# Performance work log

Measured on AMD Instinct MI355X. Metric: run time of the kernel, lower is better.

The kernel has to match this reference:

```python
import jax, jax.numpy as jnp
import numpy as np

DIM = 64
WIDTH = 128
INPUT_DIM = 16
N_NODES = 50000
N_EDGES = 100000
N_GRAPHS = 2500
STEPS = 5


def setup_inputs() -> dict:
    key = jax.random.key(0)
    ks = jax.random.split(key, 24)
    d = DIM
    def nrm(i, shape, fan_in):
        return jax.random.normal(ks[i], shape, jnp.float32) / np.float32(np.sqrt(fan_in))
    return {
        "x": jax.random.normal(ks[0], (N_NODES, INPUT_DIM - 1), jnp.float32),
        "z": jax.random.normal(ks[1], (N_NODES,), jnp.float32),
        "edge_attr": jax.random.uniform(ks[2], (N_EDGES, 5), jnp.float32),
        "lin0_w": nrm(3, (INPUT_DIM, d), INPUT_DIM),
        "lin0_b": jnp.zeros((d,), jnp.float32),
        "emlp_w1": nrm(4, (5, WIDTH), 5),
        "emlp_b1": jnp.zeros((WIDTH,), jnp.float32),
        "emlp_w2": nrm(5, (WIDTH, d * d), WIDTH),
        "emlp_b2": jnp.zeros((d * d,), jnp.float32),
        "conv_root": nrm(6, (d, d), d),
        "conv_bias": jnp.zeros((d,), jnp.float32),
        "gru_wi": nrm(7, (3 * d, d), d),
        "gru_wh": nrm(8, (3 * d, d), d),
        "gru_bi": jnp.zeros((3 * d,), jnp.float32),
        "gru_bh": jnp.zeros((3 * d,), jnp.float32),
        "lstm_wi": nrm(9, (4 * d, 2 * d), 2 * d),
        "lstm_wh": nrm(10, (4 * d, d), d),
        "lstm_bi": jnp.zeros((4 * d,), jnp.float32),
        "lstm_bh": jnp.zeros((4 * d,), jnp.float32),
        "lin1_w": nrm(11, (2 * d, d), 2 * d),
        "lin1_b": jnp.zeros((d,), jnp.float32),
        "lin2_w": nrm(12, (d, 1), d),
        "lin2_b": jnp.zeros((1,), jnp.float32),
        "edge_index": jax.random.randint(ks[13], (2, N_EDGES), 0, N_NODES),
        "batch": jnp.sort(jax.random.randint(ks[14], (N_NODES,), 0, N_GRAPHS)),
        "num_graphs": N_GRAPHS,
    }


def reference(x, z, edge_attr, lin0_w, lin0_b, emlp_w1, emlp_b1, emlp_w2, emlp_b2,
              conv_root, conv_bias, gru_wi, gru_wh, gru_bi, gru_bh,
              lstm_wi, lstm_wh, lstm_bi, lstm_bh, lin1_w, lin1_b, lin2_w, lin2_b,
              edge_index, batch, num_graphs):
    d = lin0_w.shape[1]
    n = x.shape[0]
    src, dst = edge_index[0], edge_index[1]
    # lin0 on [x | z]
    out = jax.nn.relu(jnp.concatenate([x, z[:, None]], axis=-1) @ lin0_w + lin0_b)  # [N, d]
    h = out
    # edge MLP -> per-edge weight matrix [E, d, d] (edge_attr fixed, compute once)
    ew = (jax.nn.relu(edge_attr @ emlp_w1 + emlp_b1) @ emlp_w2 + emlp_b2).reshape(-1, d, d)
    deg = jax.ops.segment_sum(jnp.ones_like(src, jnp.float32), dst, num_segments=n)
    denom = jnp.maximum(deg, 1.0)[:, None]
    for _ in range(STEPS):
        # NNConv: gather-matmul-scatter(mean) + root transform + bias
        msg = jnp.einsum('ei,eio->eo', out[src], ew)  # [E, d]
        aggr = jax.ops.segment_sum(msg, dst, num_segments=n) / denom
        m = jax.nn.relu(aggr + out @ conv_root + conv_bias)
        # GRU cell (torch gate order r, z, n)
        gi = m @ gru_wi.T + gru_bi
        gh = h @ gru_wh.T + gru_bh
        i_r, i_z, i_n = jnp.split(gi, 3, axis=-1)
        h_r, h_z, h_n = jnp.split(gh, 3, axis=-1)
        r = jax.nn.sigmoid(i_r + h_r)
        zg = jax.nn.sigmoid(i_z + h_z)
        ng = jnp.tanh(i_n + r * h_n)
        h = (1.0 - zg) * ng + zg * h
        out = h
    # Set2Set pooling (LSTM(2d -> d), torch gate order i, f, g, o)
    B = num_graphs
    q_star = jnp.zeros((B, 2 * d), out.dtype)
    hh = jnp.zeros((B, d), out.dtype)
    cc = jnp.zeros((B, d), out.dtype)
    for _ in range(STEPS):
        g = q_star @ lstm_wi.T + lstm_bi + hh @ lstm_wh.T + lstm_bh
        gi_, gf_, gg_, go_ = jnp.split(g, 4, axis=-1)
        cc = jax.nn.sigmoid(gf_) * cc + jax.nn.sigmoid(gi_) * jnp.tanh(gg_)
        hh = jax.nn.sigmoid(go_) * jnp.tanh(cc)
        q = hh
        e = jnp.sum(out * q[batch], axis=-1)  # [N]
        emax = jax.ops.segment_max(e, batch, num_segments=B)
        a = jnp.exp(e - emax[batch])
        asum = jax.ops.segment_sum(a, batch, num_segments=B) + 1e-16
        a = a / asum[batch]
        r_pool = jax.ops.segment_sum(a[:, None] * out, batch, num_segments=B)  # [B, d]
        q_star = jnp.concatenate([q, r_pool], axis=-1)
    y = jax.nn.relu(q_star @ lin1_w + lin1_b) @ lin2_w + lin2_b
    return y.reshape(-1)
```

## Files before the change

kernel.cpp:

```cpp
#include <hip/hip_runtime.h>
#include <hip/hip_bf16.h>

#define NN 50000
#define NE 100000
#define NG 2500
#define WW 128
#define EPAD 100096
#define KCH 264

typedef _Float16 h8 __attribute__((ext_vector_type(8)));
typedef _Float16 h4 __attribute__((ext_vector_type(4)));
typedef float    f4 __attribute__((ext_vector_type(4)));

#define GLOAD_LDS16(g, l) __builtin_amdgcn_global_load_lds( \
    (const __attribute__((address_space(1))) void*)(g),     \
    (__attribute__((address_space(3))) void*)(l), 16, 0, 0)

__device__ __forceinline__ float sigf(float x) { return 1.0f / (1.0f + __expf(-x)); }

__global__ void k_zero4(float4* __restrict__ p, int n4) {
    int i = blockIdx.x * 256 + threadIdx.x;
    if (i < n4) p[i] = make_float4(0.f, 0.f, 0.f, 0.f);
}

__global__ void k_transpose(float* dst, const float* src, int rows, int cols) {
    int idx = blockIdx.x * 256 + threadIdx.x;
    if (idx >= rows * cols) return;
    int r = idx / cols, c = idx % cols;
    dst[c * rows + r] = src[idx];
}

__global__ void k_lin0(const float* __restrict__ x, const float* __restrict__ z,
                       const float* __restrict__ w, const float* __restrict__ b,
                       float* __restrict__ s) {
    int idx = blockIdx.x * 256 + threadIdx.x;
    int n = idx >> 6, o = idx & 63;
    float acc = b[o];
#pragma unroll
    for (int i = 0; i < 15; i++) acc += x[n * 15 + i] * w[i * 64 + o];
    acc += z[n] * w[15 * 64 + o];
    s[idx] = fmaxf(acc, 0.0f);
}

__global__ void k_deg(const int* __restrict__ dstI, float* __restrict__ deg) {
    int e = blockIdx.x * 256 + threadIdx.x;
    if (e < NE) atomicAdd(&deg[dstI[e]], 1.0f);
}

__global__ void k_s16(const float* __restrict__ s, _Float16* __restrict__ s16) {
    int i = blockIdx.x * 256 + threadIdx.x;
    float4 v = ((const float4*)s)[i];
    h4 o = { (_Float16)v.x, (_Float16)v.y, (_Float16)v.z, (_Float16)v.w };
    *((h4*)s16 + i) = o;
}

__global__ void k_gstart(const int* __restrict__ batch, int* __restrict__ gstart) {
    int n = blockIdx.x * 256 + threadIdx.x;
    if (n > NN) return;
    int b1 = (n < NN) ? batch[n] : NG;
    int b0 = (n == 0) ? -1 : batch[n - 1];
    for (int g = b0 + 1; g <= b1; g++) gstart[g] = n;
}

__global__ void k_emlp_t(const float* __restrict__ ea, const float* __restrict__ w1,
                         const float* __restrict__ b1, _Float16* __restrict__ hidT) {
    __shared__ _Float16 hl[132][64];
    int t = threadIdx.x;
    int e0 = blockIdx.x * 64;
    int e_l = t & 63, w = t >> 6;
    int e = e0 + e_l;
    float a0 = 0, a1 = 0, a2 = 0, a3 = 0, a4 = 0;
    if (e < NE) {
        a0 = ea[e * 5 + 0]; a1 = ea[e * 5 + 1]; a2 = ea[e * 5 + 2];
        a3 = ea[e * 5 + 3]; a4 = ea[e * 5 + 4];
    }
    for (int h = w * 32; h < w * 32 + 32; h++) {
        float acc = b1[h];
        acc += a0 * w1[0 * 128 + h] + a1 * w1[1 * 128 + h] + a2 * w1[2 * 128 + h]
             + a3 * w1[3 * 128 + h] + a4 * w1[4 * 128 + h];
        hl[h][e_l] = (_Float16)fmaxf(acc, 0.0f);
    }
    if (t < 64) hl[128][t] = (_Float16)1.0f;
    else if (t < 128) hl[129][t - 64] = (_Float16)0.0f;
    else if (t < 192) hl[130][t - 128] = (_Float16)0.0f;
    else hl[131][t - 192] = (_Float16)0.0f;
    __syncthreads();
#pragma unroll
    for (int it = 0; it < 33; it++) {
        int idx = it * 256 + t;
        int h = idx >> 6, el = idx & 63;
        hidT[(size_t)h * EPAD + e0 + el] = hl[h][el];
    }
}

__global__ void k_prep_B(const float* __restrict__ w2, const float* __restrict__ b2,
                         _Float16* __restrict__ Bp) {
    int g = blockIdx.x * 256 + threadIdx.x;
    int l = g & 63, tt = (g >> 6) & 3, c = g >> 8;
    int n = tt * 16 + (l & 15);
    int kb = c * 32 + (l >> 4) * 8;
    h8 v;
#pragma unroll
    for (int j = 0; j < 8; j++) {
        int k = kb + j;
        float f = 0.0f;
        if (k < 8192) f = w2[(size_t)k * 64 + n];
        else if (k < 8256) f = b2[(k - 8192) * 64 + n];
        v[j] = (_Float16)f;
    }
    *((h8*)Bp + g) = v;
}

__global__ void k_prep_W(const float* __restrict__ conv_root,
                         const float* __restrict__ gru_wi,
                         const float* __restrict__ gru_wh,
                         _Float16* __restrict__ Bw) {
    int g = blockIdx.x * 256 + threadIdx.x;
    if (g >= 56 * 64) return;
    int l = g & 63, unit = g >> 6;
    int kb = ((unit & 1) * 32) + (l >> 4) * 8;
    h8 v;
    if (unit < 8) {
        int nt = unit >> 1;
        int n = nt * 16 + (l & 15);
#pragma unroll
        for (int j = 0; j < 8; j++) v[j] = (_Float16)conv_root[(kb + j) * 64 + n];
    } else if (unit < 32) {
        int nt = (unit - 8) >> 1;
        int o = nt * 16 + (l & 15);
#pragma unroll
        for (int j = 0; j < 8; j++) v[j] = (_Float16)gru_wi[o * 64 + kb + j];
    } else {
        int nt = (unit - 32) >> 1;
        int o = nt * 16 + (l & 15);
#pragma unroll
        for (int j = 0; j < 8; j++) v[j] = (_Float16)gru_wh[o * 64 + kb + j];
    }
    *((h8*)Bw + g) = v;
}

__global__ __launch_bounds__(128, 2) void k_fused(
        const _Float16* __restrict__ s16, const _Float16* __restrict__ hidT,
        const _Float16* __restrict__ Bp, const int* __restrict__ srcI,
        const int* __restrict__ dstI, float* __restrict__ aggr) {
    __shared__ uint4 Bl[2048];
    __shared__ _Float16 hle[128][4];
    int t = threadIdx.x, w = t >> 6, lane = t & 63;
    int m = lane & 15, q = lane >> 4;
    int e_blk = blockIdx.x * 128;
    int ew0 = e_blk + w * 64;

    h8 sA[4][2];
#pragma unroll
    for (int mt = 0; mt < 4; mt++) {
        int e = ew0 + mt * 16 + m;
        int src = (e < NE) ? srcI[e] : 0;
        const _Float16* sp = s16 + (size_t)src * 64;
        sA[mt][0] = *(const h8*)(sp + q * 8);
        sA[mt][1] = *(const h8*)(sp + 32 + q * 8);
    }
    f4 acc[4][4];
#pragma unroll
    for (int mt = 0; mt < 4; mt++)
#pragma unroll
        for (int nt = 0; nt < 4; nt++) acc[mt][nt] = (f4){0.f, 0.f, 0.f, 0.f};

    for (int sc = 0; sc < 33; sc++) {
        __syncthreads();
        const uint4* bsrc = (const uint4*)Bp + (size_t)sc * 2048;
#pragma unroll
        for (int r = 0; r < 16; r++) {
            int idx = r * 128 + t;
            GLOAD_LDS16(bsrc + idx, Bl + idx);
        }
        {
            const _Float16* hp = hidT + (size_t)(sc * 4) * EPAD + e_blk + t;
            h4 hv4;
            hv4[0] = hp[0];
            hv4[1] = hp[EPAD];
            hv4[2] = hp[2 * (size_t)EPAD];
            hv4[3] = hp[3 * (size_t)EPAD];
            *(h4*)&hle[t][0] = hv4;
        }
        __syncthreads();
        h4 hf[4];
#pragma unroll
        for (int mt = 0; mt < 4; mt++)
            hf[mt] = *(const h4*)&hle[w * 64 + mt * 16 + m][0];
#pragma unroll
        for (int cc = 0; cc < 8; cc++) {
            h8 b0 = *(const h8*)&Bl[(cc * 4 + 0) * 64 + lane];
            h8 b1 = *(const h8*)&Bl[(cc * 4 + 1) * 64 + lane];
            h8 b2 = *(const h8*)&Bl[(cc * 4 + 2) * 64 + lane];
            h8 b3 = *(const h8*)&Bl[(cc * 4 + 3) * 64 + lane];
            int hi = cc >> 1, kh = cc & 1;
#pragma unroll
            for (int mt = 0; mt < 4; mt++) {
                h8 a = sA[mt][kh] * hf[mt][hi];
                acc[mt][0] = __builtin_amdgcn_mfma_f32_16x16x32_f16(a, b0, acc[mt][0], 0, 0, 0);
                acc[mt][1] = __builtin_amdgcn_mfma_f32_16x16x32_f16(a, b1, acc[mt][1], 0, 0, 0);
                acc[mt][2] = __builtin_amdgcn_mfma_f32_16x16x32_f16(a, b2, acc[mt][2], 0, 0, 0);
                acc[mt][3] = __builtin_amdgcn_mfma_f32_16x16x32_f16(a, b3, acc[mt][3], 0, 0, 0);
            }
        }
    }
#pragma unroll
    for (int mt = 0; mt < 4; mt++) {
        int eb = ew0 + mt * 16 + q * 4;
#pragma unroll
        for (int r = 0; r < 4; r++) {
            int e = eb + r;
            if (e < NE) {
                int d = dstI[e];
                float* ap = aggr + (size_t)d * 64 + m;
                atomicAdd(ap + 0,  acc[mt][0][r]);
                atomicAdd(ap + 16, acc[mt][1][r]);
                atomicAdd(ap + 32, acc[mt][2][r]);
                atomicAdd(ap + 48, acc[mt][3][r]);
            }
        }
    }
}

__global__ __launch_bounds__(256) void k_combine2(
        float* __restrict__ s, _Float16* __restrict__ s16,
        const float* __restrict__ aggr, const float* __restrict__ deg,
        const _Float16* __restrict__ Bw, const float* __restrict__ cb,
        const float* __restrict__ bi, const float* __restrict__ bh) {
    __shared__ _Float16 ml[4][16][72];
    int t = threadIdx.x, w = t >> 6, lane = t & 63;
    int m = lane & 15, q = lane >> 4;
    int nb = blockIdx.x * 64 + w * 16;

    h8 sa0, sa1;
    {
        int node = nb + m; if (node >= NN) node = NN - 1;
        const _Float16* sp = s16 + (size_t)node * 64;
        sa0 = *(const h8*)(sp + q * 8);
        sa1 = *(const h8*)(sp + 32 + q * 8);
    }
    const h8* BW = (const h8*)Bw;

    f4 X[4], GH[12];
#pragma unroll
    for (int nt = 0; nt < 4; nt++) {
        X[nt] = (f4){0.f, 0.f, 0.f, 0.f};
        X[nt] = __builtin_amdgcn_mfma_f32_16x16x32_f16(sa0, BW[(nt * 2 + 0) * 64 + lane], X[nt], 0, 0, 0);
        X[nt] = __builtin_amdgcn_mfma_f32_16x16x32_f16(sa1, BW[(nt * 2 + 1) * 64 + lane], X[nt], 0, 0, 0);
    }
#pragma unroll
    for (int nt = 0; nt < 12; nt++) {
        GH[nt] = (f4){0.f, 0.f, 0.f, 0.f};
        GH[nt] = __builtin_amdgcn_mfma_f32_16x16x32_f16(sa0, BW[(32 + nt * 2 + 0) * 64 + lane], GH[nt], 0, 0, 0);
        GH[nt] = __builtin_amdgcn_mfma_f32_16x16x32_f16(sa1, BW[(32 + nt * 2 + 1) * 64 + lane], GH[nt], 0, 0, 0);
    }
#pragma unroll
    for (int r = 0; r < 4; r++) {
        int node = nb + q * 4 + r; if (node >= NN) node = NN - 1;
        float dn = fmaxf(deg[node], 1.0f);
#pragma unroll
        for (int nt = 0; nt < 4; nt++) {
            int o = nt * 16 + m;
            float mv = X[nt][r] + aggr[(size_t)node * 64 + o] / dn + cb[o];
            ml[w][q * 4 + r][o] = (_Float16)fmaxf(mv, 0.0f);
        }
    }
    __syncthreads();
    h8 ma0 = *(const h8*)&ml[w][m][q * 8];
    h8 ma1 = *(const h8*)&ml[w][m][32 + q * 8];

    f4 GI[12];
#pragma unroll
    for (int nt = 0; nt < 12; nt++) {
        GI[nt] = (f4){0.f, 0.f, 0.f, 0.f};
        GI[nt] = __builtin_amdgcn_mfma_f32_16x16x32_f16(ma0, BW[(8 + nt * 2 + 0) * 64 + lane], GI[nt], 0, 0, 0);
        GI[nt] = __builtin_amdgcn_mfma_f32_16x16x32_f16(ma1, BW[(8 + nt * 2 + 1) * 64 + lane], GI[nt], 0, 0, 0);
    }
#pragma unroll
    for (int og = 0; og < 4; og++) {
        int o = og * 16 + m;
        float bir = bi[o],       bhr = bh[o];
        float biz = bi[64 + o],  bhz = bh[64 + o];
        float bin = bi[128 + o], bhn = bh[128 + o];
#pragma unroll
        for (int r = 0; r < 4; r++) {
            int node = nb + q * 4 + r;
            if (node >= NN) continue;
            float rr = sigf(GI[og][r] + bir + GH[og][r] + bhr);
            float zz = sigf(GI[4 + og][r] + biz + GH[4 + og][r] + bhz);
            float ng = tanhf(GI[8 + og][r] + bin + rr * (GH[8 + og][r] + bhn));
            float hold = s[(size_t)node * 64 + o];
            float hnew = (1.0f - zz) * ng + zz * hold;
            s[(size_t)node * 64 + o] = hnew;
            s16[(size_t)node * 64 + o] = (_Float16)hnew;
        }
    }
}

__global__ void k_s2s(float* __restrict__ q_star, float* __restrict__ hh,
                      float* __restrict__ cc, const float* __restrict__ LiT,
                      const float* __restrict__ LhT, const float* __restrict__ bi,
                      const float* __restrict__ bh, const float* __restrict__ s,
                      const int* __restrict__ gstart, float* __restrict__ e_v) {
    __shared__ float qs[128], hv[64], g[256], qn[64];
    int b = blockIdx.x, t = threadIdx.x;
    if (t < 128) qs[t] = q_star[b * 128 + t];
    else if (t < 192) hv[t - 128] = hh[b * 64 + t - 128];
    __syncthreads();
    float acc = bi[t] + bh[t];
    for (int k = 0; k < 128; k++) acc += qs[k] * LiT[k * 256 + t];
    for (int k = 0; k < 64; k++) acc += hv[k] * LhT[k * 256 + t];
    g[t] = acc;
    __syncthreads();
    if (t < 64) {
        float c_new = sigf(g[64 + t]) * cc[b * 64 + t] + sigf(g[t]) * tanhf(g[128 + t]);
        cc[b * 64 + t] = c_new;
        float hq = sigf(g[192 + t]) * tanhf(c_new);
        hh[b * 64 + t] = hq;
        qn[t] = hq;
        q_star[b * 128 + t] = hq;
    }
    __syncthreads();
    if (t >= 64) return;
    int o = t;
    int n0 = gstart[b], n1 = gstart[b + 1];
    float q = qn[o];
    float mx = -3.4e38f;
    for (int n = n0; n < n1; n++) {
        float v = s[(size_t)n * 64 + o] * q;
#pragma unroll
        for (int off = 32; off; off >>= 1) v += __shfl_xor(v, off, 64);
        if (o == 0) e_v[n] = v;
        mx = fmaxf(mx, v);
    }
    float asum = 0.0f, rp = 0.0f;
    for (int n = n0; n < n1; n++) {
        float a = __expf(e_v[n] - mx);
        asum += a;
        rp += a * s[(size_t)n * 64 + o];
    }
    q_star[b * 128 + 64 + o] = rp / (asum + 1e-16f);
}

__global__ void k_final(const float* __restrict__ q_star, const float* __restrict__ w1,
                        const float* __restrict__ b1, const float* __restrict__ w2,
                        const float* __restrict__ b2, float* __restrict__ y) {
    __shared__ float qs[128];
    int b = blockIdx.x, t = threadIdx.x;
    qs[t] = q_star[b * 128 + t];
    qs[64 + t] = q_star[b * 128 + 64 + t];
    __syncthreads();
    float acc = b1[t];
    for (int k = 0; k < 128; k++) acc += qs[k] * w1[k * 64 + t];
    float hid = fmaxf(acc, 0.0f) * w2[t];
#pragma unroll
    for (int off = 32; off; off >>= 1) hid += __shfl_down(hid, off, 64);
    if (t == 0) y[b] = hid + b2[0];
}

static inline void zero_f(float* p, size_t nfloats, hipStream_t stream) {
    int n4 = (int)(nfloats / 4);
    k_zero4<<<(n4 + 255) / 256, 256, 0, stream>>>((float4*)p, n4);
}

extern "C" void kernel_launch(void* const* d_in, const int* in_sizes, int n_in,
                              void* d_out, int out_size, void* d_ws, size_t ws_size,
                              hipStream_t stream) {
    const float* x       = (const float*)d_in[0];
    const float* z       = (const float*)d_in[1];
    const float* ea      = (const float*)d_in[2];
    const float* lin0_w  = (const float*)d_in[3];
    const float* lin0_b  = (const float*)d_in[4];
    const float* emlp_w1 = (const float*)d_in[5];
    const float* emlp_b1 = (const float*)d_in[6];
    const float* emlp_w2 = (const float*)d_in[7];
    const float* emlp_b2 = (const float*)d_in[8];
    const float* conv_r  = (const float*)d_in[9];
    const float* conv_b  = (const float*)d_in[10];
    const float* gru_wi  = (const float*)d_in[11];
    const float* gru_wh  = (const float*)d_in[12];
    const float* gru_bi  = (const float*)d_in[13];
    const float* gru_bh  = (const float*)d_in[14];
    const float* lstm_wi = (const float*)d_in[15];
    const float* lstm_wh = (const float*)d_in[16];
    const float* lstm_bi = (const float*)d_in[17];
    const float* lstm_bh = (const float*)d_in[18];
    const float* lin1_w  = (const float*)d_in[19];
    const float* lin1_b  = (const float*)d_in[20];
    const float* lin2_w  = (const float*)d_in[21];
    const float* lin2_b  = (const float*)d_in[22];
    const int* eidx      = (const int*)d_in[23];
    const int* batch     = (const int*)d_in[24];
    const int* srcI = eidx;
    const int* dstI = eidx + NE;
    float* y = (float*)d_out;

    char* w = (char*)d_ws;
    size_t off = 0;
    auto alloc = [&](size_t bytes) -> void* {
        void* p = w + off;
        off += (bytes + 255) & ~(size_t)255;
        return p;
    };
    float* s      = (float*)alloc((size_t)NN * 64 * 4);
    float* aggr   = (float*)alloc((size_t)NN * 64 * 4);
    float* deg    = (float*)alloc((size_t)NN * 4);
    float* e_v    = (float*)alloc((size_t)NN * 4);
    float* q_star = (float*)alloc((size_t)NG * 128 * 4);
    float* hh     = (float*)alloc((size_t)NG * 64 * 4);
    float* cc     = (float*)alloc((size_t)NG * 64 * 4);
    float* LiT    = (float*)alloc(256 * 128 * 4);
    float* LhT    = (float*)alloc(256 * 64 * 4);
    int*   gstart = (int*)alloc((size_t)(NG + 1) * 4);
    _Float16* s16 = (_Float16*)alloc((size_t)NN * 64 * 2);
    _Float16* hidT= (_Float16*)alloc((size_t)132 * EPAD * 2);
    _Float16* Bp  = (_Float16*)alloc((size_t)KCH * 4 * 64 * 8 * 2);
    _Float16* Bw  = (_Float16*)alloc((size_t)56 * 64 * 8 * 2);
    (void)ws_size;

    k_transpose<<<(256 * 128 + 255) / 256, 256, 0, stream>>>(LiT, lstm_wi, 256, 128);
    k_transpose<<<(256 * 64 + 255) / 256, 256, 0, stream>>>(LhT, lstm_wh, 256, 64);
    k_prep_W<<<14, 256, 0, stream>>>(conv_r, gru_wi, gru_wh, Bw);

    k_lin0<<<NN * 64 / 256, 256, 0, stream>>>(x, z, lin0_w, lin0_b, s);
    k_s16<<<NN * 16 / 256, 256, 0, stream>>>(s, s16);
    zero_f(deg, NN, stream);
    k_deg<<<(NE + 255) / 256, 256, 0, stream>>>(dstI, deg);
    k_gstart<<<(NN + 256) / 256, 256, 0, stream>>>(batch, gstart);
    k_emlp_t<<<EPAD / 64, 256, 0, stream>>>(ea, emlp_w1, emlp_b1, hidT);
    k_prep_B<<<KCH * 4 * 64 / 256, 256, 0, stream>>>(emlp_w2, emlp_b2, Bp);

    for (int step = 0; step < 5; step++) {
        zero_f(aggr, (size_t)NN * 64, stream);
        k_fused<<<EPAD / 128, 128, 0, stream>>>(s16, hidT, Bp, srcI, dstI, aggr);
        k_combine2<<<(NN + 63) / 64, 256, 0, stream>>>(s, s16, aggr, deg, Bw,
                                                       conv_b, gru_bi, gru_bh);
    }

    zero_f(q_star, (size_t)NG * 128 + NG * 64 + NG * 64, stream);
    for (int it = 0; it < 5; it++) {
        k_s2s<<<NG, 256, 0, stream>>>(q_star, hh, cc, LiT, LhT, lstm_bi, lstm_bh,
                                      s, gstart, e_v);
    }
    k_final<<<NG, 64, 0, stream>>>(q_star, lin1_w, lin1_b, lin2_w, lin2_b, y);
}
```

Measured before the change: 1.056 ms.

## Double-buffer edge-weight B tiles in LDS and load hidden features directly as packed h4

The fused edge-conv kernel now splits each 2048-entry B chunk into two 1024-entry halves held in a double-buffered LDS array. The next half's global-to-LDS copy is issued before computing on the current half, overlapping memory transfer with MFMA work, and one barrier per half replaces two per chunk. The edge-MLP hidden activations are stored interleaved as h4 groups of four hidden units per edge, so each lane reads its own h4 straight from global memory, prefetched one step ahead. This removes the LDS staging buffer and an extra barrier. The costs are more registers for the prefetched values and a change in the hidT layout.

```diff
diff --git a/kernel.cpp b/kernel.cpp
--- a/kernel.cpp
+++ b/kernel.cpp
@@ -63,7 +63,7 @@
 }
 
 __global__ void k_emlp_t(const float* __restrict__ ea, const float* __restrict__ w1,
-                         const float* __restrict__ b1, _Float16* __restrict__ hidT) {
+                         const float* __restrict__ b1, _Float16* __restrict__ hidT4) {
     __shared__ _Float16 hl[132][64];
     int t = threadIdx.x;
     int e0 = blockIdx.x * 64;
@@ -86,10 +86,13 @@
     else hl[131][t - 192] = (_Float16)0.0f;
     __syncthreads();
 #pragma unroll
-    for (int it = 0; it < 33; it++) {
-        int idx = it * 256 + t;
-        int h = idx >> 6, el = idx & 63;
-        hidT[(size_t)h * EPAD + e0 + el] = hl[h][el];
+    for (int it = 0; it < 9; it++) {
+        int hq = it * 4 + w;
+        if (hq < 33) {
+            h4 v = { hl[hq * 4 + 0][e_l], hl[hq * 4 + 1][e_l],
+                     hl[hq * 4 + 2][e_l], hl[hq * 4 + 3][e_l] };
+            *(h4*)(hidT4 + ((size_t)hq * EPAD + e0 + e_l) * 4) = v;
+        }
     }
 }
 
@@ -139,12 +142,28 @@
     *((h8*)Bw + g) = v;
 }
 
+#define COMPUTE_PHASE(BUF, PAIR)                                               \
+    _Pragma("unroll")                                                          \
+    for (int c2 = 0; c2 < 4; c2++) {                                           \
+        h8 b0 = *(const h8*)&Bl[BUF][(c2 * 4 + 0) * 64 + lane];                \
+        h8 b1 = *(const h8*)&Bl[BUF][(c2 * 4 + 1) * 64 + lane];                \
+        h8 b2 = *(const h8*)&Bl[BUF][(c2 * 4 + 2) * 64 + lane];                \
+        h8 b3 = *(const h8*)&Bl[BUF][(c2 * 4 + 3) * 64 + lane];                \
+        _Pragma("unroll")                                                      \
+        for (int mt = 0; mt < 4; mt++) {                                       \
+            h8 a = sA[mt][c2 & 1] * hfA[mt][(PAIR) * 2 + (c2 >> 1)];           \
+            acc[mt][0] = __builtin_amdgcn_mfma_f32_16x16x32_f16(a, b0, acc[mt][0], 0, 0, 0); \
+            acc[mt][1] = __builtin_amdgcn_mfma_f32_16x16x32_f16(a, b1, acc[mt][1], 0, 0, 0); \
+            acc[mt][2] = __builtin_amdgcn_mfma_f32_16x16x32_f16(a, b2, acc[mt][2], 0, 0, 0); \
+            acc[mt][3] = __builtin_amdgcn_mfma_f32_16x16x32_f16(a, b3, acc[mt][3], 0, 0, 0); \
+        }                                                                      \
+    }
+
 __global__ __launch_bounds__(128, 2) void k_fused(
-        const _Float16* __restrict__ s16, const _Float16* __restrict__ hidT,
+        const _Float16* __restrict__ s16, const _Float16* __restrict__ hidT4,
         const _Float16* __restrict__ Bp, const int* __restrict__ srcI,
         const int* __restrict__ dstI, float* __restrict__ aggr) {
-    __shared__ uint4 Bl[2048];
-    __shared__ _Float16 hle[128][4];
+    __shared__ uint4 Bl[2][1024];
     int t = threadIdx.x, w = t >> 6, lane = t & 63;
     int m = lane & 15, q = lane >> 4;
     int e_blk = blockIdx.x * 128;
@@ -165,45 +184,55 @@
 #pragma unroll
         for (int nt = 0; nt < 4; nt++) acc[mt][nt] = (f4){0.f, 0.f, 0.f, 0.f};
 
-    for (int sc = 0; sc < 33; sc++) {
+    const h4* hT = (const h4*)hidT4;
+    h4 hfA[4], hfB[4];
+#pragma unroll
+    for (int mt = 0; mt < 4; mt++)
+        hfA[mt] = hT[(size_t)0 * EPAD + ew0 + mt * 16 + m];
+
+    {
+        const uint4* bs = (const uint4*)Bp;
+#pragma unroll
+        for (int r = 0; r < 8; r++) {
+            int idx = r * 128 + t;
+            GLOAD_LDS16(bs + idx, &Bl[0][idx]);
+        }
+    }
+    __syncthreads();
+
+    for (int tt = 0; tt < 33; tt++) {
+        {
+            const uint4* bs = (const uint4*)Bp + (size_t)(2 * tt + 1) * 1024;
+#pragma unroll
+            for (int r = 0; r < 8; r++) {
+                int idx = r * 128 + t;
+                GLOAD_LDS16(bs + idx, &Bl[1][idx]);
+            }
+        }
+        if (tt + 1 < 33) {
+#pragma unroll
+            for (int mt = 0; mt < 4; mt++)
+                hfB[mt] = hT[(size_t)(tt + 1) * EPAD + ew0 + mt * 16 + m];
+        }
+        COMPUTE_PHASE(0, 0)
         __syncthreads();
-        const uint4* bsrc = (const uint4*)Bp + (size_t)sc * 2048;
-#pragma unroll
-        for (int r = 0; r < 16; r++) {
-            int idx = r * 128 + t;
-            GLOAD_LDS16(bsrc + idx, Bl + idx);
-        }
-        {
-            const _Float16* hp = hidT + (size_t)(sc * 4) * EPAD + e_blk + t;
-            h4 hv4;
-            hv4[0] = hp[0];
-            hv4[1] = hp[EPAD];
-            hv4[2] = hp[2 * (size_t)EPAD];
-            hv4[3] = hp[3 * (size_t)EPAD];
-            *(h4*)&hle[t][0] = hv4;
+
+        if (tt + 1 < 33) {
+            const uint4* bs = (const uint4*)Bp + (size_t)(2 * tt + 2) * 1024;
+#pragma unroll
+            for (int r = 0; r < 8; r++) {
+                int idx = r * 128 + t;
+                GLOAD_LDS16(bs + idx, &Bl[0][idx]);
+            }
+        }
+        COMPUTE_PHASE(1, 1)
+        if (tt + 1 < 33) {
+#pragma unroll
+            for (int mt = 0; mt < 4; mt++) hfA[mt] = hfB[mt];
         }
         __syncthreads();
-        h4 hf[4];
-#pragma unroll
-        for (int mt = 0; mt < 4; mt++)
-            hf[mt] = *(const h4*)&hle[w * 64 + mt * 16 + m][0];
-#pragma unroll
-        for (int cc = 0; cc < 8; cc++) {
-            h8 b0 = *(const h8*)&Bl[(cc * 4 + 0) * 64 + lane];
-            h8 b1 = *(const h8*)&Bl[(cc * 4 + 1) * 64 + lane];
-            h8 b2 = *(const h8*)&Bl[(cc * 4 + 2) * 64 + lane];
-            h8 b3 = *(const h8*)&Bl[(cc * 4 + 3) * 64 + lane];
-            int hi = cc >> 1, kh = cc & 1;
-#pragma unroll
-            for (int mt = 0; mt < 4; mt++) {
-                h8 a = sA[mt][kh] * hf[mt][hi];
-                acc[mt][0] = __builtin_amdgcn_mfma_f32_16x16x32_f16(a, b0, acc[mt][0], 0, 0, 0);
-                acc[mt][1] = __builtin_amdgcn_mfma_f32_16x16x32_f16(a, b1, acc[mt][1], 0, 0, 0);
-                acc[mt][2] = __builtin_amdgcn_mfma_f32_16x16x32_f16(a, b2, acc[mt][2], 0, 0, 0);
-                acc[mt][3] = __builtin_amdgcn_mfma_f32_16x16x32_f16(a, b3, acc[mt][3], 0, 0, 0);
-            }
-        }
-    }
+    }
+
 #pragma unroll
     for (int mt = 0; mt < 4; mt++) {
         int eb = ew0 + mt * 16 + q * 4;
@@ -413,7 +442,7 @@
     float* LhT    = (float*)alloc(256 * 64 * 4);
     int*   gstart = (int*)alloc((size_t)(NG + 1) * 4);
     _Float16* s16 = (_Float16*)alloc((size_t)NN * 64 * 2);
-    _Float16* hidT= (_Float16*)alloc((size_t)132 * EPAD * 2);
+    _Float16* hidT= (_Float16*)alloc((size_t)33 * EPAD * 4 * 2);
     _Float16* Bp  = (_Float16*)alloc((size_t)KCH * 4 * 64 * 8 * 2);
     _Float16* Bw  = (_Float16*)alloc((size_t)56 * 64 * 8 * 2);
     (void)ws_size;
```

Result: slower. 1.095 ms (+3.7%).
